# Optimization experiments

Measured on AMD Instinct MI355X. Metric: run time of the kernel, lower is better.

The kernel has to match this reference:

```python
import jax, jax.numpy as jnp
import numpy as np

B, T = 128, 128
CONT, HID, EMB = 16, 128, 64
K, CE, VSP, VLC = 8192, 6, 2000, 32
BETA = 0.25
FUSE_IN = 3 * HID  # naip_rep + cont_h + cat_h, each HID wide


def setup_inputs() -> dict:
    key = jax.random.key(0)
    ks = jax.random.split(key, 40)

    def w(i, shape):
        return jax.random.normal(ks[i], shape, dtype=jnp.float32) * 0.05

    return {
        'cont': jax.random.normal(ks[0], (B, T, CONT), dtype=jnp.float32),
        'naip': jax.random.normal(ks[1], (B, 1, 3, 3), dtype=jnp.float32),
        'cat': jax.random.randint(ks[2], (B, T, 2), 0, VLC, dtype=jnp.int32),
        # encoder params
        'cat_emb_sp': w(3, (VSP, CE)),
        'cat_emb_lc': w(4, (VLC, CE)),
        'conv_w': w(5, (HID, 1, 3, 3)), 'conv_b': w(6, (HID,)),
        'naip_proj_w': w(7, (HID, HID)), 'naip_proj_b': w(8, (HID,)),
        'cont_proj_w': w(9, (HID, CONT)), 'cont_proj_b': w(10, (HID,)),
        'cat_proj_w': w(11, (HID, 2 * CE)), 'cat_proj_b': w(12, (HID,)),
        'fuse1_w': w(13, (HID, FUSE_IN)), 'fuse1_b': w(14, (HID,)),
        'fuse2_w': w(15, (EMB, HID)), 'fuse2_b': w(16, (EMB,)),
        # quantizer
        'codebook': w(17, (K, EMB)),
        # decoder params
        'bb1_w': w(18, (HID, EMB)), 'bb1_b': w(19, (HID,)),
        'bb2_w': w(20, (HID, HID)), 'bb2_b': w(21, (HID,)),
        'cont_head_w': w(22, (CONT, HID)), 'cont_head_b': w(23, (CONT,)),
        'sp_head_w': w(24, (VSP, HID)), 'sp_head_b': w(25, (VSP,)),
        'lc_head_w': w(26, (VLC, HID)), 'lc_head_b': w(27, (VLC,)),
        'can1_w': w(28, (HID, HID)), 'can1_b': w(29, (HID,)),
        'can2_w': w(30, (1, HID)), 'can2_b': w(31, (1,)),
    }


def lin(x, w, b):
    return x @ w.T + b


def reference(cont, naip, cat, cat_emb_sp, cat_emb_lc, conv_w, conv_b,
              naip_proj_w, naip_proj_b, cont_proj_w, cont_proj_b,
              cat_proj_w, cat_proj_b, fuse1_w, fuse1_b, fuse2_w, fuse2_b,
              codebook, bb1_w, bb1_b, bb2_w, bb2_b, cont_head_w, cont_head_b,
              sp_head_w, sp_head_b, lc_head_w, lc_head_b,
              can1_w, can1_b, can2_w, can2_b):
    # ---- encoder ----
    naip = jnp.nan_to_num(naip, nan=0.0, posinf=0.0, neginf=0.0)
    # Conv2d(k=3) on a 3x3 patch == full contraction -> [B, HID]
    naip_feat = jax.nn.relu(jnp.einsum('bchw,ochw->bo', naip, conv_w) + conv_b)
    naip_feat = lin(naip_feat, naip_proj_w, naip_proj_b)          # [B, HID]
    naip_rep = jnp.broadcast_to(naip_feat[:, None, :], (B, T, HID))

    cont_h = lin(jnp.nan_to_num(cont, nan=0.0, posinf=0.0, neginf=0.0),
                 cont_proj_w, cont_proj_b)                        # [B, T, HID]

    cat_concat = jnp.concatenate([cat_emb_sp[cat[..., 0]],
                                  cat_emb_lc[cat[..., 1]]], axis=-1)  # [B,T,2*CE]
    cat_h = lin(cat_concat, cat_proj_w, cat_proj_b)               # [B, T, HID]

    fused = jnp.concatenate([naip_rep, cont_h, cat_h], axis=-1)   # [B, T, 3*HID]
    z_e = lin(jax.nn.relu(lin(fused, fuse1_w, fuse1_b)), fuse2_w, fuse2_b)  # [B,T,EMB]

    # ---- ST vector quantizer ----
    z = z_e.reshape(-1, EMB)                                       # [N, EMB]
    z_sq = jnp.sum(z * z, axis=1, keepdims=True)                   # [N, 1]
    e_sq = jnp.sum(codebook * codebook, axis=1)                    # [K]
    distances = z_sq + e_sq[None, :] - 2.0 * (z @ codebook.T)      # [N, K]
    indices = jnp.argmin(distances, axis=1)                        # [N]
    z_q = codebook[indices].reshape(z_e.shape)                     # [B, T, EMB]

    commitment = jnp.mean((jax.lax.stop_gradient(z_e) - z_q) ** 2)
    codebook_l = jnp.mean((z_e - jax.lax.stop_gradient(z_q)) ** 2)
    loss_vq = codebook_l + BETA * commitment
    z_q_st = z_e + jax.lax.stop_gradient(z_q - z_e)

    counts = jnp.bincount(indices, length=K).astype(jnp.float32)
    avg_probs = counts / indices.shape[0]
    perplexity = jnp.exp(-jnp.sum(avg_probs * jnp.log(avg_probs + 1e-12)))

    # ---- decoder ----
    h = jax.nn.relu(lin(jax.nn.relu(lin(z_q_st, bb1_w, bb1_b)), bb2_w, bb2_b))  # [B,T,HID]
    cont_rec = lin(h, cont_head_w, cont_head_b)                    # [B, T, CONT]
    sp_logits = lin(h, sp_head_w, sp_head_b)                       # [B, T, VSP]
    lc_logits = lin(h, lc_head_w, lc_head_b)                       # [B, T, VLC]
    h_last = h[:, -1, :]
    canopy = jnp.squeeze(lin(jax.nn.relu(lin(h_last, can1_w, can1_b)), can2_w, can2_b), -1)  # [B]

    return (cont_rec, sp_logits, lc_logits, canopy,
            indices.reshape(B, T), loss_vq, perplexity)
```

## Files before the change

### kernel.cpp

```cpp
#include <hip/hip_runtime.h>
#include <cmath>

namespace {
constexpr int Bn = 128, Tn = 128, BTn = Bn * Tn;
constexpr int CONTn = 16, HIDn = 128, EMBn = 64;
constexpr int Kn = 8192, CEn = 6, VSPn = 2000, VLCn = 32, FINn = 3 * HIDn;
constexpr int VSP_PAD = 2048;
constexpr int CAP = 128;
constexpr float EPSC = 0.02f;
constexpr int KCH = 128;
constexpr int NCH = Kn / KCH;
constexpr int TOKB = 32;

constexpr size_t WS_NAIP2 = 0;
constexpr size_t WS_ZE    = WS_NAIP2 + (size_t)Bn * HIDn;
constexpr size_t WS_ZQ    = WS_ZE + (size_t)BTn * EMBn;
constexpr size_t WS_H     = WS_ZQ + (size_t)BTn * EMBn;
constexpr size_t WS_ESQ   = WS_H + (size_t)BTn * HIDn;
constexpr size_t WS_PART  = WS_ESQ + Kn;
constexpr size_t WS_CNTK  = WS_PART + BTn / 4;
constexpr size_t WS_CNTT  = WS_CNTK + Kn;
constexpr size_t WS_Q     = WS_CNTT + BTn;
constexpr size_t WS_CAND  = WS_Q + BTn;
constexpr size_t WS_ZBF   = WS_CAND + (size_t)BTn * CAP;
constexpr size_t WS_CBBF  = WS_ZBF + (size_t)BTn * EMBn / 2;
constexpr size_t WS_HBF   = WS_CBBF + (size_t)Kn * EMBn / 2;
constexpr size_t WS_WBF   = WS_HBF + (size_t)BTn * HIDn / 2;
constexpr size_t WS_RCG   = WS_WBF + (size_t)VSP_PAD * HIDn / 2;

constexpr size_t O_CONT = 0;
constexpr size_t O_SP   = O_CONT + (size_t)BTn * CONTn;
constexpr size_t O_LC   = O_SP + (size_t)BTn * VSPn;
constexpr size_t O_CAN  = O_LC + (size_t)BTn * VLCn;
constexpr size_t O_IDX  = O_CAN + Bn;
constexpr size_t O_LOSS = O_IDX + BTn;
constexpr size_t O_PPL  = O_LOSS + 1;
}

typedef __attribute__((ext_vector_type(8))) short short8v;
typedef __attribute__((ext_vector_type(4))) float f32x4;

__device__ __forceinline__ float nan0(float v) {
    return __builtin_isfinite(v) ? v : 0.0f;
}
__device__ __forceinline__ float dot4(float4 a, float4 b) {
    return a.x * b.x + a.y * b.y + a.z * b.z + a.w * b.w;
}
__device__ __forceinline__ unsigned short f2bf(float f) {
    union { float f; unsigned u; } v{f};
    unsigned r = v.u + 0x7FFFu + ((v.u >> 16) & 1u);
    return (unsigned short)(r >> 16);
}
__device__ __forceinline__ unsigned fenc(float f) {
    unsigned b = __float_as_uint(f);
    return (b & 0x80000000u) ? ~b : (b | 0x80000000u);
}
__device__ __forceinline__ float fdec(unsigned k) {
    unsigned b = (k >> 31) ? (k & 0x7fffffffu) : ~k;
    return __uint_as_float(b);
}

__global__ __launch_bounds__(256) void k_esq_zero(const float* __restrict__ cb,
                                                  float* __restrict__ e_sq,
                                                  int* __restrict__ counts,
                                                  unsigned short* __restrict__ cbbf) {
    int i = blockIdx.x * 256 + threadIdx.x;
    if (i < Kn) {
        counts[i] = 0;
        const float4* r = (const float4*)(cb + (size_t)i * EMBn);
        float s = 0.f;
#pragma unroll
        for (int j = 0; j < 16; ++j) {
            float4 v = r[j];
            s += dot4(v, v);
            unsigned short u[4] = {f2bf(v.x), f2bf(v.y), f2bf(v.z), f2bf(v.w)};
            *(uint2*)(cbbf + (size_t)i * EMBn + j * 4) = *(const uint2*)u;
        }
        e_sq[i] = s;
    }
}

__global__ __launch_bounds__(256) void k_rcmax(const float* __restrict__ e_sq,
                                               float* __restrict__ rcg) {
    const int tid = threadIdx.x;
    float m = 0.f;
#pragma unroll
    for (int j = 0; j < Kn / 256; ++j) m = fmaxf(m, e_sq[j * 256 + tid]);
#pragma unroll
    for (int off = 32; off > 0; off >>= 1) m = fmaxf(m, __shfl_xor(m, off));
    __shared__ float wm[4];
    if ((tid & 63) == 0) wm[tid >> 6] = m;
    __syncthreads();
    if (tid == 0)
        rcg[0] = sqrtf(fmaxf(fmaxf(wm[0], wm[1]), fmaxf(wm[2], wm[3]))) * 1.000001f;
}

__global__ __launch_bounds__(256) void k_wcast(const float* __restrict__ w,
                                               unsigned short* __restrict__ wbf) {
    int i = blockIdx.x * 256 + threadIdx.x;
    int v = i >> 5;
    unsigned short u[4] = {0, 0, 0, 0};
    if (v < VSPn) {
        float4 x = ((const float4*)w)[i];
        u[0] = f2bf(x.x); u[1] = f2bf(x.y); u[2] = f2bf(x.z); u[3] = f2bf(x.w);
    }
    *(uint2*)(wbf + (size_t)i * 4) = *(const uint2*)u;
}

__global__ __launch_bounds__(128) void k_naip(const float* __restrict__ naip,
                                              const float* __restrict__ conv_w,
                                              const float* __restrict__ conv_b,
                                              const float* __restrict__ pw,
                                              const float* __restrict__ pb,
                                              float* __restrict__ naip2) {
    int b = blockIdx.x, o = threadIdx.x;
    __shared__ float feat[HIDn];
    float acc = conv_b[o];
#pragma unroll
    for (int i = 0; i < 9; ++i) acc += nan0(naip[b * 9 + i]) * conv_w[o * 9 + i];
    feat[o] = fmaxf(acc, 0.f);
    __syncthreads();
    float a2 = pb[o];
    const float4* wr = (const float4*)(pw + (size_t)o * HIDn);
    const float4* fr = (const float4*)feat;
#pragma unroll
    for (int j = 0; j < 32; ++j) a2 += dot4(fr[j], wr[j]);
    naip2[(size_t)b * HIDn + o] = a2;
}

__global__ __launch_bounds__(256) void k_ze(
    const float* __restrict__ cont, const int* __restrict__ cat,
    const float* __restrict__ emb_sp, const float* __restrict__ emb_lc,
    const float* __restrict__ cpw, const float* __restrict__ cpb,
    const float* __restrict__ caw, const float* __restrict__ cab,
    const float* __restrict__ f1w, const float* __restrict__ f1b,
    const float* __restrict__ f2w, const float* __restrict__ f2b,
    const float* __restrict__ naip2, float* __restrict__ z_e) {
    const int tok0 = blockIdx.x * 16;
    const int tid = threadIdx.x;
    __shared__ float fused[16][FINn + 4];
    __shared__ float h1[16][HIDn + 4];

    for (int idx = tid; idx < 16 * HIDn; idx += 256) {
        int t = idx >> 7, j = idx & 127;
        int b = (tok0 + t) / Tn;
        fused[t][j] = naip2[(size_t)b * HIDn + j];
    }
    for (int idx = tid; idx < 16 * HIDn; idx += 256) {
        int t = idx >> 7, o = idx & 127;
        int tok = tok0 + t;
        const float4* cp = (const float4*)(cont + (size_t)tok * CONTn);
        const float4* wr = (const float4*)(cpw + (size_t)o * CONTn);
        float a = cpb[o];
#pragma unroll
        for (int q = 0; q < 4; ++q) {
            float4 c4 = cp[q], w4 = wr[q];
            a += nan0(c4.x) * w4.x + nan0(c4.y) * w4.y + nan0(c4.z) * w4.z + nan0(c4.w) * w4.w;
        }
        fused[t][HIDn + o] = a;
    }
    for (int idx = tid; idx < 16 * HIDn; idx += 256) {
        int t = idx >> 7, o = idx & 127;
        int tok = tok0 + t;
        int c0 = cat[tok * 2], c1 = cat[tok * 2 + 1];
        const float* e0 = emb_sp + (size_t)c0 * CEn;
        const float* e1 = emb_lc + (size_t)c1 * CEn;
        const float* wr = caw + (size_t)o * (2 * CEn);
        float a = cab[o];
#pragma unroll
        for (int i = 0; i < CEn; ++i) a += e0[i] * wr[i];
#pragma unroll
        for (int i = 0; i < CEn; ++i) a += e1[i] * wr[CEn + i];
        fused[t][2 * HIDn + o] = a;
    }
    __syncthreads();
    {
        int o = tid >> 1, half = tid & 1;
        float acc[8];
        float bv = f1b[o];
#pragma unroll
        for (int t = 0; t < 8; ++t) acc[t] = bv;
        const float4* wr = (const float4*)(f1w + (size_t)o * FINn);
        for (int kk = 0; kk < FINn / 4; ++kk) {
            float4 w = wr[kk];
#pragma unroll
            for (int t = 0; t < 8; ++t) {
                float4 f = ((const float4*)&fused[half * 8 + t][0])[kk];
                acc[t] += dot4(f, w);
            }
        }
#pragma unroll
        for (int t = 0; t < 8; ++t) h1[half * 8 + t][o] = fmaxf(acc[t], 0.f);
    }
    __syncthreads();
    {
        int o = tid & 63, tg = tid >> 6;
        float acc[4];
        float bv = f2b[o];
#pragma unroll
        for (int t = 0; t < 4; ++t) acc[t] = bv;
        const float4* wr = (const float4*)(f2w + (size_t)o * HIDn);
        for (int kk = 0; kk < HIDn / 4; ++kk) {
            float4 w = wr[kk];
#pragma unroll
            for (int t = 0; t < 4; ++t) {
                float4 f = ((const float4*)&h1[tg * 4 + t][0])[kk];
                acc[t] += dot4(f, w);
            }
        }
#pragma unroll
        for (int t = 0; t < 4; ++t) z_e[(size_t)(tok0 + tg * 4 + t) * EMBn + o] = acc[t];
    }
}

__global__ __launch_bounds__(256) void k_zprep(const float* __restrict__ z_e,
                                               unsigned short* __restrict__ zbf,
                                               float* __restrict__ qtok) {
    const int lane = threadIdx.x & 63;
    const int tg = threadIdx.x >> 6;
    const int t = blockIdx.x * 4 + tg;
    float zv = z_e[(size_t)t * EMBn + lane];
    zbf[(size_t)t * EMBn + lane] = f2bf(zv);
    float s = zv * zv;
#pragma unroll
    for (int off = 32; off > 0; off >>= 1) s += __shfl_xor(s, off);
    if (lane == 0) qtok[t] = EPSC * sqrtf(s);
}

__device__ __forceinline__ void vq_stage(unsigned char* dst,
                                         const unsigned short* __restrict__ gsrc,
                                         int tid) {
#pragma unroll
    for (int it = 0; it < 4; ++it) {
        int c16 = it * 256 + tid;
        int row = c16 >> 3, col16 = c16 & 7;
        short8v v = *(const short8v*)(gsrc + (size_t)c16 * 8);
        *(short8v*)(dst + row * 128 + ((col16 ^ (row & 7)) << 4)) = v;
    }
}

__global__ __launch_bounds__(256, 4) void k_vq_sweep(
    const unsigned short* __restrict__ zbf, const unsigned short* __restrict__ cbbf,
    const float* __restrict__ e_sq, const float* __restrict__ qtok,
    const float* __restrict__ rcg,
    int* __restrict__ cntT, int* __restrict__ cand) {
    const int tid = threadIdx.x;
    const int lane = tid & 63;
    const int wid = tid >> 6;
    const int lrow = lane & 15;
    const int g = lane >> 4;
    const int tok0 = blockIdx.x * TOKB;

    __shared__ __align__(16) unsigned char bufA[KCH * 128];
    __shared__ __align__(16) unsigned char bufB[KCH * 128];
    __shared__ unsigned tauL[TOKB];
    __shared__ int cntL[TOKB];

    if (tid < TOKB) { tauL[tid] = 0u; cntL[tid] = 0; }

    short8v bz[2][2];
#pragma unroll
    for (int n = 0; n < 2; ++n)
#pragma unroll
        for (int kc = 0; kc < 2; ++kc)
            bz[n][kc] = *(const short8v*)(zbf + (size_t)(tok0 + n * 16 + lrow) * EMBn + kc * 32 + g * 8);
    float qn[2];
#pragma unroll
    for (int n = 0; n < 2; ++n) qn[n] = qtok[tok0 + n * 16 + lrow];
    const float rcm = rcg[0];

    vq_stage(bufA, cbbf, tid);
    __syncthreads();

    for (int c = 0; c < NCH; ++c) {
        const unsigned char* cur = (c & 1) ? bufB : bufA;
        unsigned char* nxt = (c & 1) ? bufA : bufB;
        if (c + 1 < NCH) vq_stage(nxt, cbbf + (size_t)(c + 1) * KCH * EMBn, tid);

        const int cw = c * KCH + wid * 32;
        float4 e0 = *(const float4*)(e_sq + cw + g * 4);
        float4 e1 = *(const float4*)(e_sq + cw + 16 + g * 4);

        f32x4 acc[2][2];
        {
            f32x4 em0 = {-0.5f * e0.x, -0.5f * e0.y, -0.5f * e0.z, -0.5f * e0.w};
            f32x4 em1 = {-0.5f * e1.x, -0.5f * e1.y, -0.5f * e1.z, -0.5f * e1.w};
#pragma unroll
            for (int n = 0; n < 2; ++n) { acc[0][n] = em0; acc[1][n] = em1; }
        }
#pragma unroll
        for (int kc = 0; kc < 2; ++kc)
#pragma unroll
            for (int m = 0; m < 2; ++m) {
                const int row = wid * 32 + m * 16 + lrow;
                short8v ac = *(const short8v*)(
                    cur + row * 128 + ((((kc << 2) + g) ^ (row & 7)) << 4));
#pragma unroll
                for (int n = 0; n < 2; ++n)
                    acc[m][n] = __builtin_amdgcn_mfma_f32_16x16x32_bf16(ac, bz[n][kc], acc[m][n], 0, 0, 0);
            }

#pragma unroll
        for (int n = 0; n < 2; ++n) {
            float v = fmaxf(fmaxf(fmaxf(acc[0][n][0], acc[0][n][1]), fmaxf(acc[0][n][2], acc[0][n][3])),
                            fmaxf(fmaxf(acc[1][n][0], acc[1][n][1]), fmaxf(acc[1][n][2], acc[1][n][3])));
            v = fmaxf(v, __shfl_xor(v, 16));
            v = fmaxf(v, __shfl_xor(v, 32));
            if (lane < 16) atomicMax(&tauL[n * 16 + lane], fenc(v));
        }
        __syncthreads();

#pragma unroll
        for (int n = 0; n < 2; ++n) {
            float tf = fdec(tauL[n * 16 + lrow]);
            float nthr = tf - qn[n] * rcm;
#pragma unroll
            for (int m = 0; m < 2; ++m)
#pragma unroll
                for (int r = 0; r < 4; ++r)
                    if (acc[m][n][r] >= nthr) {
                        const int tn = n * 16 + lrow;
                        int slot = atomicAdd(&cntL[tn], 1);
                        if (slot < CAP)
                            cand[(size_t)(tok0 + tn) * CAP + slot] = cw + m * 16 + g * 4 + r;
                    }
        }
    }
    __syncthreads();
    if (tid < TOKB) cntT[tok0 + tid] = cntL[tid];
}

__global__ __launch_bounds__(256) void k_vq_rescore(
    const int* __restrict__ cntT, const int* __restrict__ cand,
    const float* __restrict__ z_e, const float* __restrict__ cb,
    const float* __restrict__ e_sq,
    float* __restrict__ z_q, float* __restrict__ idx_out,
    int* __restrict__ counts, float* __restrict__ partials) {
    const int lane = threadIdx.x & 63;
    const int tg = threadIdx.x >> 6;
    const int t = blockIdx.x * 4 + tg;
    __shared__ float psum[4];

    float4 z[16];
    const float4* zr = (const float4*)(z_e + (size_t)t * EMBn);
#pragma unroll
    for (int q = 0; q < 16; ++q) z[q] = zr[q];

    const int n = cntT[t];
    float best = INFINITY;
    int bi = Kn;

    if (n > 0 && n <= CAP) {
        for (int s = lane; s < n; s += 64) {
            int c = cand[(size_t)t * CAP + s];
            const float4* cp = (const float4*)(cb + (size_t)c * EMBn);
            float a = 0.f;
#pragma unroll
            for (int q = 0; q < 16; ++q) a += dot4(z[q], cp[q]);
            float d = e_sq[c] - 2.f * a;
            if (d < best || (d == best && c < bi)) { best = d; bi = c; }
        }
    } else {
        for (int c0 = 0; c0 < Kn; c0 += 64) {
            int c = c0 + lane;
            const float4* cp = (const float4*)(cb + (size_t)c * EMBn);
            float a = 0.f;
#pragma unroll
            for (int q = 0; q < 16; ++q) a += dot4(z[q], cp[q]);
            float d = e_sq[c] - 2.f * a;
            if (d < best) { best = d; bi = c; }
        }
    }
#pragma unroll
    for (int off = 32; off > 0; off >>= 1) {
        float od = __shfl_xor(best, off);
        int oi = __shfl_xor(bi, off);
        if (od < best || (od == best && oi < bi)) { best = od; bi = oi; }
    }

    float cv = cb[(size_t)bi * EMBn + lane];
    z_q[(size_t)t * EMBn + lane] = cv;
    float zv = z_e[(size_t)t * EMBn + lane];
    float diff = zv - cv;
    float s = diff * diff;
#pragma unroll
    for (int off = 32; off > 0; off >>= 1) s += __shfl_xor(s, off);
    if (lane == 0) {
        psum[tg] = s;
        idx_out[t] = (float)bi;
        atomicAdd(&counts[bi], 1);
    }
    __syncthreads();
    if (threadIdx.x == 0) partials[blockIdx.x] = psum[0] + psum[1] + psum[2] + psum[3];
}

__global__ __launch_bounds__(256) void k_backbone(
    const float* __restrict__ z_q,
    const float* __restrict__ bb1w, const float* __restrict__ bb1b,
    const float* __restrict__ bb2w, const float* __restrict__ bb2b,
    const float* __restrict__ chw, const float* __restrict__ chb,
    const float* __restrict__ lcw, const float* __restrict__ lcb,
    float* __restrict__ h_out, unsigned short* __restrict__ hbf_out,
    float* __restrict__ cont_rec, float* __restrict__ lc_out) {
    const int tid = threadIdx.x;
    const int tok0 = blockIdx.x * 16;
    __shared__ float zq[16][68];
    __shared__ float h1[16][HIDn + 4];
    __shared__ float h2[16][HIDn + 4];
    {
        int t = tid >> 4, q = tid & 15;
        ((float4*)&zq[t][0])[q] = ((const float4*)(z_q + (size_t)(tok0 + t) * EMBn))[q];
    }
    __syncthreads();
    {
        int o = tid >> 1, half = tid & 1;
        float acc[8];
        float bv = bb1b[o];
#pragma unroll
        for (int t = 0; t < 8; ++t) acc[t] = bv;
        const float4* wr = (const float4*)(bb1w + (size_t)o * EMBn);
#pragma unroll
        for (int kk = 0; kk < 16; ++kk) {
            float4 w = wr[kk];
#pragma unroll
            for (int t = 0; t < 8; ++t) acc[t] += dot4(((const float4*)&zq[half * 8 + t][0])[kk], w);
        }
#pragma unroll
        for (int t = 0; t < 8; ++t) h1[half * 8 + t][o] = fmaxf(acc[t], 0.f);
    }
    __syncthreads();
    {
        int o = tid >> 1, half = tid & 1;
        float acc[8];
        float bv = bb2b[o];
#pragma unroll
        for (int t = 0; t < 8; ++t) acc[t] = bv;
        const float4* wr = (const float4*)(bb2w + (size_t)o * HIDn);
        for (int kk = 0; kk < 32; ++kk) {
            float4 w = wr[kk];
#pragma unroll
            for (int t = 0; t < 8; ++t) acc[t] += dot4(((const float4*)&h1[half * 8 + t][0])[kk], w);
        }
#pragma unroll
        for (int t = 0; t < 8; ++t) {
            float v = fmaxf(acc[t], 0.f);
            h2[half * 8 + t][o] = v;
            h_out[(size_t)(tok0 + half * 8 + t) * HIDn + o] = v;
            hbf_out[(size_t)(tok0 + half * 8 + t) * HIDn + o] = f2bf(v);
        }
    }
    __syncthreads();
    {
        int t = tid >> 4, o = tid & 15;
        float a = chb[o];
        const float4* wr = (const float4*)(chw + (size_t)o * HIDn);
#pragma unroll
        for (int kk = 0; kk < 32; ++kk) a += dot4(((const float4*)&h2[t][0])[kk], wr[kk]);
        cont_rec[(size_t)(tok0 + t) * CONTn + o] = a;
    }
    for (int idx = tid; idx < 16 * 32; idx += 256) {
        int t = idx >> 5, o = idx & 31;
        float a = lcb[o];
        const float4* wr = (const float4*)(lcw + (size_t)o * HIDn);
#pragma unroll
        for (int kk = 0; kk < 32; ++kk) a += dot4(((const float4*)&h2[t][0])[kk], wr[kk]);
        lc_out[(size_t)(tok0 + t) * VLCn + o] = a;
    }
}

__global__ __launch_bounds__(256, 3) void k_sp_mfma(
    const unsigned short* __restrict__ hbf, const unsigned short* __restrict__ wbf,
    const float* __restrict__ bias, float* __restrict__ out) {
    const int tid = threadIdx.x;
    const int lane = tid & 63;
    const int wid = tid >> 6;
    const int tok_w = blockIdx.y * 128 + (wid & 1) * 64;
    const int v_w = blockIdx.x * 128 + (wid >> 1) * 64;

    const int lrow = lane & 15;
    const int lk = (lane >> 4) * 8;

    const unsigned short* ha = hbf + (size_t)(tok_w + lrow) * HIDn + lk;
    const unsigned short* wa = wbf + (size_t)(v_w + lrow) * HIDn + lk;

    f32x4 acc[4][4];
#pragma unroll
    for (int m = 0; m < 4; ++m)
#pragma unroll
        for (int n = 0; n < 4; ++n) acc[m][n] = (f32x4){0.f, 0.f, 0.f, 0.f};

#pragma unroll
    for (int ks = 0; ks < 4; ++ks) {
        const int kk = ks * 32;
        short8v a[4], b[4];
#pragma unroll
        for (int m = 0; m < 4; ++m)
            a[m] = *(const short8v*)(ha + (size_t)m * 16 * HIDn + kk);
#pragma unroll
        for (int n = 0; n < 4; ++n)
            b[n] = *(const short8v*)(wa + (size_t)n * 16 * HIDn + kk);
#pragma unroll
        for (int m = 0; m < 4; ++m)
#pragma unroll
            for (int n = 0; n < 4; ++n)
                acc[m][n] = __builtin_amdgcn_mfma_f32_16x16x32_bf16(a[m], b[n], acc[m][n], 0, 0, 0);
    }

    const int r0 = (lane >> 4) * 4;
#pragma unroll
    for (int n = 0; n < 4; ++n) {
        const int col = v_w + n * 16 + lrow;
        if (col < VSPn) {
            const float bv = bias[col];
#pragma unroll
            for (int m = 0; m < 4; ++m) {
                const int row = tok_w + m * 16 + r0;
#pragma unroll
                for (int r = 0; r < 4; ++r)
                    out[(size_t)(row + r) * VSPn + col] = acc[m][n][r] + bv;
            }
        }
    }
}

__global__ __launch_bounds__(128) void k_canopy(const float* __restrict__ h,
                                                const float* __restrict__ w1,
                                                const float* __restrict__ b1,
                                                const float* __restrict__ w2,
                                                const float* __restrict__ b2,
                                                float* __restrict__ can) {
    int b = blockIdx.x, o = threadIdx.x;
    __shared__ float r[128];
    const float4* hr = (const float4*)(h + (size_t)(b * Tn + Tn - 1) * HIDn);
    const float4* wr = (const float4*)(w1 + (size_t)o * HIDn);
    float a = b1[o];
#pragma unroll
    for (int kk = 0; kk < 32; ++kk) a += dot4(hr[kk], wr[kk]);
    r[o] = fmaxf(a, 0.f) * w2[o];
    __syncthreads();
    for (int s = 64; s > 0; s >>= 1) {
        if (o < s) r[o] += r[o + s];
        __syncthreads();
    }
    if (o == 0) can[b] = r[0] + b2[0];
}

__global__ __launch_bounds__(256) void k_finalize(const float* __restrict__ partials,
                                                  const int* __restrict__ counts,
                                                  float* __restrict__ out_loss,
                                                  float* __restrict__ out_ppl) {
    const int tid = threadIdx.x;
    __shared__ float red[256];
    float ps = 0.f;
#pragma unroll
    for (int j = 0; j < (BTn / 4) / 256; ++j) ps += partials[tid * ((BTn / 4) / 256) + j];
    red[tid] = ps;
    __syncthreads();
    for (int s = 128; s > 0; s >>= 1) {
        if (tid < s) red[tid] += red[tid + s];
        __syncthreads();
    }
    float total = red[0];
    __syncthreads();
    float e = 0.f;
    for (int i = tid; i < Kn; i += 256) {
        float p = (float)counts[i] * (1.0f / BTn);
        e += p * logf(p + 1e-12f);
    }
    red[tid] = e;
    __syncthreads();
    for (int s = 128; s > 0; s >>= 1) {
        if (tid < s) red[tid] += red[tid + s];
        __syncthreads();
    }
    if (tid == 0) {
        out_loss[0] = 1.25f * total / (float)((size_t)BTn * EMBn);
        out_ppl[0] = expf(-red[0]);
    }
}

extern "C" void kernel_launch(void* const* d_in, const int* in_sizes, int n_in,
                              void* d_out, int out_size, void* d_ws, size_t ws_size,
                              hipStream_t stream) {
    const float* cont = (const float*)d_in[0];
    const float* naip = (const float*)d_in[1];
    const int* cat = (const int*)d_in[2];
    const float* emb_sp = (const float*)d_in[3];
    const float* emb_lc = (const float*)d_in[4];
    const float* conv_w = (const float*)d_in[5];
    const float* conv_b = (const float*)d_in[6];
    const float* npw = (const float*)d_in[7];
    const float* npb = (const float*)d_in[8];
    const float* cpw = (const float*)d_in[9];
    const float* cpb = (const float*)d_in[10];
    const float* caw = (const float*)d_in[11];
    const float* cab = (const float*)d_in[12];
    const float* f1w = (const float*)d_in[13];
    const float* f1b = (const float*)d_in[14];
    const float* f2w = (const float*)d_in[15];
    const float* f2b = (const float*)d_in[16];
    const float* cb = (const float*)d_in[17];
    const float* bb1w = (const float*)d_in[18];
    const float* bb1b = (const float*)d_in[19];
    const float* bb2w = (const float*)d_in[20];
    const float* bb2b = (const float*)d_in[21];
    const float* chw = (const float*)d_in[22];
    const float* chb = (const float*)d_in[23];
    const float* spw = (const float*)d_in[24];
    const float* spb = (const float*)d_in[25];
    const float* lcw = (const float*)d_in[26];
    const float* lcb = (const float*)d_in[27];
    const float* c1w = (const float*)d_in[28];
    const float* c1b = (const float*)d_in[29];
    const float* c2w = (const float*)d_in[30];
    const float* c2b = (const float*)d_in[31];

    float* out = (float*)d_out;
    float* ws = (float*)d_ws;
    float* naip2 = ws + WS_NAIP2;
    float* z_e = ws + WS_ZE;
    float* z_q = ws + WS_ZQ;
    float* h = ws + WS_H;
    float* e_sq = ws + WS_ESQ;
    float* parts = ws + WS_PART;
    int* counts = (int*)(ws + WS_CNTK);
    int* cntT = (int*)(ws + WS_CNTT);
    float* qtok = ws + WS_Q;
    int* cand = (int*)(ws + WS_CAND);
    unsigned short* zbf = (unsigned short*)(ws + WS_ZBF);
    unsigned short* cbbf = (unsigned short*)(ws + WS_CBBF);
    unsigned short* hbf = (unsigned short*)(ws + WS_HBF);
    unsigned short* wbf = (unsigned short*)(ws + WS_WBF);
    float* rcg = ws + WS_RCG;

    k_esq_zero<<<dim3(Kn / 256), dim3(256), 0, stream>>>(cb, e_sq, counts, cbbf);
    k_rcmax<<<dim3(1), dim3(256), 0, stream>>>(e_sq, rcg);
    k_wcast<<<dim3(VSP_PAD * HIDn / 4 / 256), dim3(256), 0, stream>>>(spw, wbf);
    k_naip<<<dim3(Bn), dim3(128), 0, stream>>>(naip, conv_w, conv_b, npw, npb, naip2);
    k_ze<<<dim3(BTn / 16), dim3(256), 0, stream>>>(cont, cat, emb_sp, emb_lc, cpw, cpb, caw, cab,
                                                   f1w, f1b, f2w, f2b, naip2, z_e);
    k_zprep<<<dim3(BTn / 4), dim3(256), 0, stream>>>(z_e, zbf, qtok);
    k_vq_sweep<<<dim3(BTn / TOKB), dim3(256), 0, stream>>>(zbf, cbbf, e_sq, qtok, rcg, cntT, cand);
    k_vq_rescore<<<dim3(BTn / 4), dim3(256), 0, stream>>>(cntT, cand, z_e, cb, e_sq, z_q,
                                                          out + O_IDX, counts, parts);
    k_backbone<<<dim3(BTn / 16), dim3(256), 0, stream>>>(z_q, bb1w, bb1b, bb2w, bb2b, chw, chb,
                                                         lcw, lcb, h, hbf, out + O_CONT, out + O_LC);
    k_sp_mfma<<<dim3(VSP_PAD / 128, BTn / 128), dim3(256), 0, stream>>>(hbf, wbf, spb, out + O_SP);
    k_canopy<<<dim3(Bn), dim3(128), 0, stream>>>(h, c1w, c1b, c2w, c2b, out + O_CAN);
    k_finalize<<<dim3(1), dim3(256), 0, stream>>>(parts, counts, out + O_LOSS, out + O_PPL);
}
```

Before: 326.9 us.

## Drop LDS staging and per-chunk barriers in VQ sweep, load codebook directly

```diff
diff --git a/kernel.cpp b/kernel.cpp
--- a/kernel.cpp
+++ b/kernel.cpp
@@ -8,9 +8,9 @@
 constexpr int VSP_PAD = 2048;
 constexpr int CAP = 128;
 constexpr float EPSC = 0.02f;
-constexpr int KCH = 128;
-constexpr int NCH = Kn / KCH;
 constexpr int TOKB = 32;
+constexpr int KCW = 64;
+constexpr int NIT = Kn / (KCW * 8);
 
 constexpr size_t WS_NAIP2 = 0;
 constexpr size_t WS_ZE    = WS_NAIP2 + (size_t)Bn * HIDn;
@@ -227,19 +227,7 @@
     if (lane == 0) qtok[t] = EPSC * sqrtf(s);
 }
 
-__device__ __forceinline__ void vq_stage(unsigned char* dst,
-                                         const unsigned short* __restrict__ gsrc,
-                                         int tid) {
-#pragma unroll
-    for (int it = 0; it < 4; ++it) {
-        int c16 = it * 256 + tid;
-        int row = c16 >> 3, col16 = c16 & 7;
-        short8v v = *(const short8v*)(gsrc + (size_t)c16 * 8);
-        *(short8v*)(dst + row * 128 + ((col16 ^ (row & 7)) << 4)) = v;
-    }
-}
-
-__global__ __launch_bounds__(256, 4) void k_vq_sweep(
+__global__ __launch_bounds__(512, 4) void k_vq_sweep(
     const unsigned short* __restrict__ zbf, const unsigned short* __restrict__ cbbf,
     const float* __restrict__ e_sq, const float* __restrict__ qtok,
     const float* __restrict__ rcg,
@@ -251,11 +239,8 @@
     const int g = lane >> 4;
     const int tok0 = blockIdx.x * TOKB;
 
-    __shared__ __align__(16) unsigned char bufA[KCH * 128];
-    __shared__ __align__(16) unsigned char bufB[KCH * 128];
     __shared__ unsigned tauL[TOKB];
     __shared__ int cntL[TOKB];
-
     if (tid < TOKB) { tauL[tid] = 0u; cntL[tid] = 0; }
 
     short8v bz[2][2];
@@ -268,61 +253,55 @@
 #pragma unroll
     for (int n = 0; n < 2; ++n) qn[n] = qtok[tok0 + n * 16 + lrow];
     const float rcm = rcg[0];
-
-    vq_stage(bufA, cbbf, tid);
-    __syncthreads();
-
-    for (int c = 0; c < NCH; ++c) {
-        const unsigned char* cur = (c & 1) ? bufB : bufA;
-        unsigned char* nxt = (c & 1) ? bufA : bufB;
-        if (c + 1 < NCH) vq_stage(nxt, cbbf + (size_t)(c + 1) * KCH * EMBn, tid);
-
-        const int cw = c * KCH + wid * 32;
-        float4 e0 = *(const float4*)(e_sq + cw + g * 4);
-        float4 e1 = *(const float4*)(e_sq + cw + 16 + g * 4);
-
-        f32x4 acc[2][2];
-        {
-            f32x4 em0 = {-0.5f * e0.x, -0.5f * e0.y, -0.5f * e0.z, -0.5f * e0.w};
-            f32x4 em1 = {-0.5f * e1.x, -0.5f * e1.y, -0.5f * e1.z, -0.5f * e1.w};
-#pragma unroll
-            for (int n = 0; n < 2; ++n) { acc[0][n] = em0; acc[1][n] = em1; }
+    __syncthreads();
+
+    for (int it = 0; it < NIT; ++it) {
+        const int c0 = (it * 8 + wid) * KCW;
+        short8v ac[4][2];
+        float4 e4[4];
+#pragma unroll
+        for (int m = 0; m < 4; ++m) {
+#pragma unroll
+            for (int kc = 0; kc < 2; ++kc)
+                ac[m][kc] = *(const short8v*)(cbbf + (size_t)(c0 + m * 16 + lrow) * EMBn + kc * 32 + g * 8);
+            e4[m] = *(const float4*)(e_sq + c0 + m * 16 + g * 4);
+        }
+        f32x4 acc[4][2];
+#pragma unroll
+        for (int m = 0; m < 4; ++m) {
+            f32x4 em = {-0.5f * e4[m].x, -0.5f * e4[m].y, -0.5f * e4[m].z, -0.5f * e4[m].w};
+            acc[m][0] = em;
+            acc[m][1] = em;
         }
 #pragma unroll
         for (int kc = 0; kc < 2; ++kc)
 #pragma unroll
-            for (int m = 0; m < 2; ++m) {
-                const int row = wid * 32 + m * 16 + lrow;
-                short8v ac = *(const short8v*)(
-                    cur + row * 128 + ((((kc << 2) + g) ^ (row & 7)) << 4));
+            for (int m = 0; m < 4; ++m)
 #pragma unroll
                 for (int n = 0; n < 2; ++n)
-                    acc[m][n] = __builtin_amdgcn_mfma_f32_16x16x32_bf16(ac, bz[n][kc], acc[m][n], 0, 0, 0);
-            }
+                    acc[m][n] = __builtin_amdgcn_mfma_f32_16x16x32_bf16(ac[m][kc], bz[n][kc], acc[m][n], 0, 0, 0);
 
 #pragma unroll
         for (int n = 0; n < 2; ++n) {
-            float v = fmaxf(fmaxf(fmaxf(acc[0][n][0], acc[0][n][1]), fmaxf(acc[0][n][2], acc[0][n][3])),
-                            fmaxf(fmaxf(acc[1][n][0], acc[1][n][1]), fmaxf(acc[1][n][2], acc[1][n][3])));
+            float v = acc[0][n][0];
+#pragma unroll
+            for (int m = 0; m < 4; ++m)
+#pragma unroll
+                for (int r = 0; r < 4; ++r) v = fmaxf(v, acc[m][n][r]);
             v = fmaxf(v, __shfl_xor(v, 16));
             v = fmaxf(v, __shfl_xor(v, 32));
             if (lane < 16) atomicMax(&tauL[n * 16 + lane], fenc(v));
-        }
-        __syncthreads();
-
-#pragma unroll
-        for (int n = 0; n < 2; ++n) {
-            float tf = fdec(tauL[n * 16 + lrow]);
+            float tf = fmaxf(fdec(tauL[n * 16 + lrow]), v);
             float nthr = tf - qn[n] * rcm;
-#pragma unroll
-            for (int m = 0; m < 2; ++m)
+            const int tn = n * 16 + lrow;
+#pragma unroll
+            for (int m = 0; m < 4; ++m)
 #pragma unroll
                 for (int r = 0; r < 4; ++r)
                     if (acc[m][n][r] >= nthr) {
-                        const int tn = n * 16 + lrow;
                         int slot = atomicAdd(&cntL[tn], 1);
                         if (slot < CAP)
-                            cand[(size_t)(tok0 + tn) * CAP + slot] = cw + m * 16 + g * 4 + r;
+                            cand[(size_t)(tok0 + tn) * CAP + slot] = c0 + m * 16 + g * 4 + r;
                     }
         }
     }
@@ -640,7 +619,7 @@
     k_ze<<<dim3(BTn / 16), dim3(256), 0, stream>>>(cont, cat, emb_sp, emb_lc, cpw, cpb, caw, cab,
                                                    f1w, f1b, f2w, f2b, naip2, z_e);
     k_zprep<<<dim3(BTn / 4), dim3(256), 0, stream>>>(z_e, zbf, qtok);
-    k_vq_sweep<<<dim3(BTn / TOKB), dim3(256), 0, stream>>>(zbf, cbbf, e_sq, qtok, rcg, cntT, cand);
+    k_vq_sweep<<<dim3(BTn / TOKB), dim3(512), 0, stream>>>(zbf, cbbf, e_sq, qtok, rcg, cntT, cand);
     k_vq_rescore<<<dim3(BTn / 4), dim3(256), 0, stream>>>(cntT, cand, z_e, cb, e_sq, z_q,
                                                           out + O_IDX, counts, parts);
     k_backbone<<<dim3(BTn / 16), dim3(256), 0, stream>>>(z_q, bb1w, bb1b, bb2w, bb2b, chw, chb,
```

Measured after the change: 309.2 us, median of 2. -5.4%, faster.
